# Optimization experiments

Hardware: AMD Instinct MI355X
Metric: run time of the kernel (lower is better)

The kernel has to match this reference:

```python
import jax, jax.numpy as jnp
import numpy as np

NUM_HEADS = 8
MESSAGE_DIM = 256
ATT_DIM = MESSAGE_DIM // NUM_HEADS  # 32
NUM_NODES = 100000
NUM_EDGES = 1600000
NEG_SLOPE = 0.1


def setup_inputs() -> dict:
    key = jax.random.key(0)
    k1, k2, k3, k4, k5 = jax.random.split(key, 5)
    source = jax.random.randint(k1, (NUM_EDGES,), 0, NUM_NODES)
    target = jax.random.randint(k2, (NUM_EDGES,), 0, NUM_NODES)
    message = jax.random.normal(k3, (NUM_EDGES, MESSAGE_DIM), dtype=jnp.float32)
    x_e = jax.random.normal(k4, (NUM_NODES, MESSAGE_DIM), dtype=jnp.float32)
    # xavier_uniform for shape (num_heads, 2*att_dim): fan_in=2*att_dim, fan_out=num_heads
    fan_in, fan_out = 2 * ATT_DIM, NUM_HEADS
    limit = float(np.sqrt(6.0 / (fan_in + fan_out)))
    weight = jax.random.uniform(k5, (NUM_HEADS, 2 * ATT_DIM), minval=-limit, maxval=limit, dtype=jnp.float32)
    return {"source": source, "target": target, "message": message, "x_e": x_e, "weight": weight}


def reference(source, target, message, x_e, weight):
    E = message.shape[0]
    N = x_e.shape[0]
    H, two_d = weight.shape
    D = two_d // 2
    m = message.reshape(E, H, D)                 # (E,H,D)
    xt = x_e[target].reshape(E, H, D)            # gather target node states
    feat = jnp.concatenate([m, xt], axis=-1)     # (E,H,2D)
    score = jnp.einsum("ehd,hd->eh", feat, weight)
    alpha = jnp.where(score >= 0, score, NEG_SLOPE * score)  # LeakyReLU(0.1)
    # scatter-softmax over edges grouped by target node
    mx = jax.ops.segment_max(alpha, target, num_segments=N)  # (N,H)
    ex = jnp.exp(alpha - mx[target])
    s = jax.ops.segment_sum(ex, target, num_segments=N)      # (N,H)
    alpha = ex / jnp.maximum(s[target], 1e-16)
    # dropout is identity in eval mode
    out = (m * alpha[:, :, None]).reshape(E, H * D)
    return out
```

## Files before the change

### kernel.cpp

```cpp
#include <hip/hip_runtime.h>
#include <math.h>

#define H 8
#define D 32

typedef float f32x4 __attribute__((ext_vector_type(4)));

__global__ void aew_init_kernel(float* __restrict__ s, int n) {
    int i = blockIdx.x * blockDim.x + threadIdx.x;
    if (i < n) s[i] = 0.0f;
}

__global__ __launch_bounds__(256) void aew_score_kernel(
    const int*   __restrict__ target,
    const float* __restrict__ message,
    const float* __restrict__ x_e,
    const float* __restrict__ weight,
    float*       __restrict__ ex,
    float*       __restrict__ s,
    int E)
{
    const int lane = threadIdx.x & 63;
    const int h = lane >> 3;
    const int j = lane & 7;
    const int wavesPerBlock = blockDim.x >> 6;
    const int wave = blockIdx.x * wavesPerBlock + (threadIdx.x >> 6);
    const int nWaves = gridDim.x * wavesPerBlock;

    const f32x4 w1 = *(const f32x4*)(weight + h * 64 + j * 4);
    const f32x4 w2 = *(const f32x4*)(weight + h * 64 + 32 + j * 4);

    for (int e = wave; e < E; e += nWaves) {
        int t = target[e];
        f32x4 mv = __builtin_nontemporal_load((const f32x4*)(message + (size_t)e * 256) + lane);
        f32x4 xv = *((const f32x4*)(x_e + (size_t)t * 256) + lane);
        float p = mv.x * w1.x + mv.y * w1.y + mv.z * w1.z + mv.w * w1.w
                + xv.x * w2.x + xv.y * w2.y + xv.z * w2.z + xv.w * w2.w;
        p += __shfl_xor(p, 1);
        p += __shfl_xor(p, 2);
        p += __shfl_xor(p, 4);
        float a = (p >= 0.0f) ? p : 0.1f * p;
        float e_a = __expf(a);
        if (j == 0) {
            ex[(size_t)e * H + h] = e_a;
            atomicAdd(&s[(size_t)t * H + h], e_a);
        }
    }
}

__global__ __launch_bounds__(256) void aew_output_kernel(
    const int*   __restrict__ target,
    const float* __restrict__ message,
    const float* __restrict__ ex,
    const float* __restrict__ s,
    float*       __restrict__ out,
    int n4)
{
    int i4 = blockIdx.x * blockDim.x + threadIdx.x;
    if (i4 >= n4) return;
    int e = i4 >> 6;
    int h = (i4 & 63) >> 3;
    int t = target[e];
    float sc = ex[e * H + h] / fmaxf(s[t * H + h], 1e-16f);
    f32x4 mv = __builtin_nontemporal_load(((const f32x4*)message) + i4);
    f32x4 o = mv * sc;
    __builtin_nontemporal_store(o, ((f32x4*)out) + i4);
}

extern "C" void kernel_launch(void* const* d_in, const int* in_sizes, int n_in,
                              void* d_out, int out_size, void* d_ws, size_t ws_size,
                              hipStream_t stream) {
    const int*   target  = (const int*)d_in[1];
    const float* message = (const float*)d_in[2];
    const float* x_e     = (const float*)d_in[3];
    const float* weight  = (const float*)d_in[4];
    float* out = (float*)d_out;

    const int E = in_sizes[1];
    const int N = in_sizes[3] / 256;
    const int NH = N * H;

    float* ex = (float*)d_ws;
    float* s  = ex + (size_t)E * H;

    aew_init_kernel<<<(NH + 255) / 256, 256, 0, stream>>>(s, NH);
    aew_score_kernel<<<2048, 256, 0, stream>>>(target, message, x_e, weight, ex, s, E);
    const int n4 = E * 64;
    aew_output_kernel<<<(n4 + 255) / 256, 256, 0, stream>>>(target, message, ex, s, out, n4);
}
```

Measured before the change: 994.2 us.

## Precompute per-node x_e·weight projections and prefetch target gather in score kernel

Adds a kernel that computes the x_e half of the attention score once per node and head (N×H values), so the score kernel gathers one float per edge-head instead of a full 256-float row of x_e per edge. This cuts the random-gather traffic from about 1KB per edge to 32 bytes per edge, at the cost of an extra launch and a small workspace array. The score loop also software-prefetches the next edge's target index and projection value to hide gather latency.

New measurement: 869.3 us (median of 2 runs). -12.6%, faster.

```diff
diff --git a/kernel.cpp b/kernel.cpp
--- a/kernel.cpp
+++ b/kernel.cpp
@@ -6,15 +6,44 @@
 
 typedef float f32x4 __attribute__((ext_vector_type(4)));
 
+__device__ __forceinline__ float dot4(f32x4 a, f32x4 b) {
+    return a.x * b.x + a.y * b.y + a.z * b.z + a.w * b.w;
+}
+
 __global__ void aew_init_kernel(float* __restrict__ s, int n) {
     int i = blockIdx.x * blockDim.x + threadIdx.x;
     if (i < n) s[i] = 0.0f;
 }
 
+__global__ __launch_bounds__(256) void aew_xw_kernel(
+    const float* __restrict__ x_e,
+    const float* __restrict__ weight,
+    float*       __restrict__ xw,
+    int N)
+{
+    const int lane = threadIdx.x & 63;
+    const int h = lane >> 3;
+    const int j = lane & 7;
+    const int wavesPerBlock = blockDim.x >> 6;
+    const int wave = blockIdx.x * wavesPerBlock + (threadIdx.x >> 6);
+    const int nWaves = gridDim.x * wavesPerBlock;
+
+    const f32x4 w2 = *(const f32x4*)(weight + h * 64 + 32 + j * 4);
+
+    for (int n = wave; n < N; n += nWaves) {
+        f32x4 xv = *((const f32x4*)(x_e + (size_t)n * 256) + lane);
+        float d = dot4(xv, w2);
+        d += __shfl_xor(d, 1);
+        d += __shfl_xor(d, 2);
+        d += __shfl_xor(d, 4);
+        if (j == 0) xw[(size_t)n * H + h] = d;
+    }
+}
+
 __global__ __launch_bounds__(256) void aew_score_kernel(
     const int*   __restrict__ target,
     const float* __restrict__ message,
-    const float* __restrict__ x_e,
+    const float* __restrict__ xw,
     const float* __restrict__ weight,
     float*       __restrict__ ex,
     float*       __restrict__ s,
@@ -28,23 +57,28 @@
     const int nWaves = gridDim.x * wavesPerBlock;
 
     const f32x4 w1 = *(const f32x4*)(weight + h * 64 + j * 4);
-    const f32x4 w2 = *(const f32x4*)(weight + h * 64 + 32 + j * 4);
 
-    for (int e = wave; e < E; e += nWaves) {
-        int t = target[e];
+    int e = wave;
+    int t = (e < E) ? target[e] : 0;
+    float xwv = (e < E) ? xw[(size_t)t * H + h] : 0.0f;
+    for (; e < E; e += nWaves) {
+        const int en = e + nWaves;
+        int tn = (en < E) ? target[en] : 0;
+        float xwn = (en < E) ? xw[(size_t)tn * H + h] : 0.0f;
+
         f32x4 mv = __builtin_nontemporal_load((const f32x4*)(message + (size_t)e * 256) + lane);
-        f32x4 xv = *((const f32x4*)(x_e + (size_t)t * 256) + lane);
-        float p = mv.x * w1.x + mv.y * w1.y + mv.z * w1.z + mv.w * w1.w
-                + xv.x * w2.x + xv.y * w2.y + xv.z * w2.z + xv.w * w2.w;
-        p += __shfl_xor(p, 1);
-        p += __shfl_xor(p, 2);
-        p += __shfl_xor(p, 4);
+        float d = dot4(mv, w1);
+        d += __shfl_xor(d, 1);
+        d += __shfl_xor(d, 2);
+        d += __shfl_xor(d, 4);
+        float p = d + xwv;
         float a = (p >= 0.0f) ? p : 0.1f * p;
-        float e_a = __expf(a);
+        float ea = __expf(a);
         if (j == 0) {
-            ex[(size_t)e * H + h] = e_a;
-            atomicAdd(&s[(size_t)t * H + h], e_a);
+            ex[(size_t)e * H + h] = ea;
+            atomicAdd(&s[(size_t)t * H + h], ea);
         }
+        t = tn; xwv = xwn;
     }
 }
 
@@ -82,9 +116,11 @@
 
     float* ex = (float*)d_ws;
     float* s  = ex + (size_t)E * H;
+    float* xw = s + (size_t)NH;
 
     aew_init_kernel<<<(NH + 255) / 256, 256, 0, stream>>>(s, NH);
-    aew_score_kernel<<<2048, 256, 0, stream>>>(target, message, x_e, weight, ex, s, E);
+    aew_xw_kernel<<<1024, 256, 0, stream>>>(x_e, weight, xw, N);
+    aew_score_kernel<<<2048, 256, 0, stream>>>(target, message, xw, weight, ex, s, E);
     const int n4 = E * 64;
     aew_output_kernel<<<(n4 + 255) / 256, 256, 0, stream>>>(target, message, ex, s, out, n4);
 }
```
